# Optimization experiments

Hardware: AMD Instinct MI355X
Metric: run time of the kernel (lower is better)

Reference implementation:

```python
import jax, jax.numpy as jnp
import numpy as np

M, N, C, D = 2, 8, 1024, 256  # n_routers, num_adapters, channel_dim, down_sample_size
B, S = 32, 512


def setup_inputs() -> dict:
    key = jax.random.key(0)
    k1, k2, k3, k4, k5 = jax.random.split(key, 5)
    x = jax.random.normal(k1, (B, S, C), dtype=jnp.float32)
    expert_index = jax.random.randint(k2, (M, B), 0, N, dtype=jnp.int32)
    down_w = jax.random.normal(k3, (M, N, C, D), dtype=jnp.float32) * 0.01
    down_b = jax.random.normal(k4, (M, N, D), dtype=jnp.float32) * 0.01
    up_w = jax.random.normal(k5, (M, N, D, C), dtype=jnp.float32) * 0.01
    return {"x": x, "expert_index": expert_index, "down_w": down_w,
            "down_b": down_b, "up_w": up_w}


def reference(x, expert_index, down_w, down_b, up_w):
    # Gather per-(router, batch-element) adapter weights along the adapter axis.
    idx = expert_index  # [M, B]
    bw_down = jnp.take_along_axis(down_w, idx[:, :, None, None], axis=1)  # [M, B, C, D]
    bb_down = jnp.take_along_axis(down_b, idx[:, :, None], axis=1)        # [M, B, D]
    bw_up = jnp.take_along_axis(up_w, idx[:, :, None, None], axis=1)      # [M, B, D, C]
    # z = swish(x @ W_down + b_down)  -> [M, B, S, D]
    z = jnp.einsum('bsc,mbcd->mbsd', x, bw_down) + bb_down[:, :, None, :]
    z = jax.nn.silu(z)
    # u = z @ W_up -> [M, B, S, C]
    u = jnp.einsum('mbsd,mbdc->mbsc', z, bw_up)
    return u
```

## Files before the change

### kernel.cpp

```cpp
#include <hip/hip_runtime.h>
#include <stdint.h>

typedef unsigned short u16;
typedef __bf16 bf16x8 __attribute__((ext_vector_type(8)));
typedef float f32x4 __attribute__((ext_vector_type(4)));

#define MM 2
#define NN 8
#define CC 1024
#define DD 256
#define BB 32
#define SS 512

__device__ __forceinline__ u16 f2bf(float f) {
  uint32_t u = __float_as_uint(f);
  u += 0x7FFFu + ((u >> 16) & 1u);
  return (u16)(u >> 16);
}

__device__ __forceinline__ void async16(const void* g, void* l) {
  __builtin_amdgcn_global_load_lds(
      (const __attribute__((address_space(1))) uint32_t*)g,
      (__attribute__((address_space(3))) uint32_t*)l, 16, 0, 0);
}

__global__ __launch_bounds__(256) void cvt_f32_bf16(
    const float* __restrict__ in, u16* __restrict__ out, int n) {
  int i = (blockIdx.x * 256 + threadIdx.x) * 4;
  if (i >= n) return;
  float4 v = *reinterpret_cast<const float4*>(in + i);
  u16 o[4] = {f2bf(v.x), f2bf(v.y), f2bf(v.z), f2bf(v.w)};
  *reinterpret_cast<uint2*>(out + i) = *reinterpret_cast<const uint2*>(o);
}

__global__ __launch_bounds__(256) void transpose_cvt(
    const float* __restrict__ in, u16* __restrict__ out, int R, int L) {
  __shared__ float tile[32][33];
  const int slab = blockIdx.z;
  const float* src = in + (size_t)slab * R * L;
  u16* dst = out + (size_t)slab * R * L;
  const int c0 = blockIdx.x * 32;
  const int r0 = blockIdx.y * 32;
  const int tx = threadIdx.x & 31, ty = threadIdx.x >> 5;
#pragma unroll
  for (int i = 0; i < 32; i += 8)
    tile[ty + i][tx] = src[(size_t)(r0 + ty + i) * L + c0 + tx];
  __syncthreads();
#pragma unroll
  for (int i = 0; i < 32; i += 8)
    dst[(size_t)(c0 + ty + i) * R + r0 + tx] = f2bf(tile[tx][ty + i]);
}

__global__ __launch_bounds__(256) void gemm_down(
    const u16* __restrict__ xb, const u16* __restrict__ wdT,
    const float* __restrict__ db, const int* __restrict__ eidx,
    u16* __restrict__ z) {
  __shared__ __align__(16) u16 smA[128 * 32];
  __shared__ __align__(16) u16 smB[128 * 32];

  const int pair = blockIdx.z;
  const int m = pair >> 5;
  const int b = pair & 31;
  const int e = eidx[pair];
  const int s0 = blockIdx.y * 128;
  const int d0 = blockIdx.x * 128;

  const int tid = threadIdx.x;
  const int lane = tid & 63;
  const int wave = tid >> 6;
  const int quad = lane >> 4;
  const int l16 = lane & 15;

  const u16* Ab = xb + ((size_t)b * SS + s0) * CC;
  const u16* Bb = wdT + ((size_t)(m * NN + e) * DD + d0) * CC;

  const int r0r = (wave * 2 + 0) * 16 + (lane >> 2);
  const int r1r = (wave * 2 + 1) * 16 + (lane >> 2);
  const int kc = (lane & 3) * 8;
  const u16* gA0 = Ab + (size_t)r0r * CC + kc;
  const u16* gA1 = Ab + (size_t)r1r * CC + kc;
  const u16* gB0 = Bb + (size_t)r0r * CC + kc;
  const u16* gB1 = Bb + (size_t)r1r * CC + kc;
  u16* lA0 = smA + (wave * 2 + 0) * 512;
  u16* lA1 = smA + (wave * 2 + 1) * 512;
  u16* lB0 = smB + (wave * 2 + 0) * 512;
  u16* lB1 = smB + (wave * 2 + 1) * 512;

  const int wr = (wave >> 1) * 64;
  const int wc = (wave & 1) * 64;

  f32x4 acc[4][4];
#pragma unroll
  for (int i = 0; i < 4; ++i)
#pragma unroll
    for (int j = 0; j < 4; ++j) acc[i][j] = (f32x4){0.f, 0.f, 0.f, 0.f};

  for (int kk = 0; kk < CC; kk += 32) {
    async16(gA0 + kk, lA0);
    async16(gA1 + kk, lA1);
    async16(gB0 + kk, lB0);
    async16(gB1 + kk, lB1);
    __syncthreads();
    bf16x8 af[4], bfr[4];
#pragma unroll
    for (int i = 0; i < 4; ++i)
      af[i] = *reinterpret_cast<const bf16x8*>(&smA[(wr + i * 16 + l16) * 32 + quad * 8]);
#pragma unroll
    for (int j = 0; j < 4; ++j)
      bfr[j] = *reinterpret_cast<const bf16x8*>(&smB[(wc + j * 16 + l16) * 32 + quad * 8]);
#pragma unroll
    for (int i = 0; i < 4; ++i)
#pragma unroll
      for (int j = 0; j < 4; ++j)
        acc[i][j] = __builtin_amdgcn_mfma_f32_16x16x32_bf16(af[i], bfr[j], acc[i][j], 0, 0, 0);
    __syncthreads();
  }

  const float* bias_p = db + (size_t)(m * NN + e) * DD + d0;
  u16* zb = z + (size_t)pair * SS * DD;
#pragma unroll
  for (int j = 0; j < 4; ++j) {
    const int dloc = wc + j * 16 + l16;
    const float bias = bias_p[dloc];
#pragma unroll
    for (int i = 0; i < 4; ++i) {
      const int srow = s0 + wr + i * 16 + quad * 4;
#pragma unroll
      for (int r = 0; r < 4; ++r) {
        float v = acc[i][j][r] + bias;
        v = v / (1.f + __expf(-v));
        zb[(size_t)(srow + r) * DD + d0 + dloc] = f2bf(v);
      }
    }
  }
}

__global__ __launch_bounds__(256) void gemm_up(
    const u16* __restrict__ zb, const u16* __restrict__ wuT,
    const int* __restrict__ eidx, float* __restrict__ out) {
  __shared__ __align__(16) u16 smA[128 * 32];
  __shared__ __align__(16) u16 smB[128 * 32];

  const int pair = blockIdx.z;
  const int m = pair >> 5;
  const int e = eidx[pair];
  const int s0 = blockIdx.y * 128;
  const int c0 = blockIdx.x * 128;

  const int tid = threadIdx.x;
  const int lane = tid & 63;
  const int wave = tid >> 6;
  const int quad = lane >> 4;
  const int l16 = lane & 15;

  const u16* Ab = zb + ((size_t)pair * SS + s0) * DD;
  const u16* Bb = wuT + ((size_t)(m * NN + e) * CC + c0) * DD;

  const int r0r = (wave * 2 + 0) * 16 + (lane >> 2);
  const int r1r = (wave * 2 + 1) * 16 + (lane >> 2);
  const int kc = (lane & 3) * 8;
  const u16* gA0 = Ab + (size_t)r0r * DD + kc;
  const u16* gA1 = Ab + (size_t)r1r * DD + kc;
  const u16* gB0 = Bb + (size_t)r0r * DD + kc;
  const u16* gB1 = Bb + (size_t)r1r * DD + kc;
  u16* lA0 = smA + (wave * 2 + 0) * 512;
  u16* lA1 = smA + (wave * 2 + 1) * 512;
  u16* lB0 = smB + (wave * 2 + 0) * 512;
  u16* lB1 = smB + (wave * 2 + 1) * 512;

  const int wr = (wave >> 1) * 64;
  const int wc = (wave & 1) * 64;

  f32x4 acc[4][4];
#pragma unroll
  for (int i = 0; i < 4; ++i)
#pragma unroll
    for (int j = 0; j < 4; ++j) acc[i][j] = (f32x4){0.f, 0.f, 0.f, 0.f};

  for (int kk = 0; kk < DD; kk += 32) {
    async16(gA0 + kk, lA0);
    async16(gA1 + kk, lA1);
    async16(gB0 + kk, lB0);
    async16(gB1 + kk, lB1);
    __syncthreads();
    bf16x8 af[4], bfr[4];
#pragma unroll
    for (int i = 0; i < 4; ++i)
      af[i] = *reinterpret_cast<const bf16x8*>(&smA[(wr + i * 16 + l16) * 32 + quad * 8]);
#pragma unroll
    for (int j = 0; j < 4; ++j)
      bfr[j] = *reinterpret_cast<const bf16x8*>(&smB[(wc + j * 16 + l16) * 32 + quad * 8]);
#pragma unroll
    for (int i = 0; i < 4; ++i)
#pragma unroll
      for (int j = 0; j < 4; ++j)
        acc[i][j] = __builtin_amdgcn_mfma_f32_16x16x32_bf16(af[i], bfr[j], acc[i][j], 0, 0, 0);
    __syncthreads();
  }

  float* ob = out + (size_t)pair * SS * CC;
#pragma unroll
  for (int j = 0; j < 4; ++j) {
    const int cloc = c0 + wc + j * 16 + l16;
#pragma unroll
    for (int i = 0; i < 4; ++i) {
      const int srow = s0 + wr + i * 16 + quad * 4;
#pragma unroll
      for (int r = 0; r < 4; ++r)
        ob[(size_t)(srow + r) * CC + cloc] = acc[i][j][r];
    }
  }
}

extern "C" void kernel_launch(void* const* d_in, const int* in_sizes, int n_in,
                              void* d_out, int out_size, void* d_ws, size_t ws_size,
                              hipStream_t stream) {
  const float* x  = (const float*)d_in[0];
  const int* eidx = (const int*)d_in[1];
  const float* dw = (const float*)d_in[2];
  const float* db = (const float*)d_in[3];
  const float* uw = (const float*)d_in[4];
  float* out = (float*)d_out;

  char* ws = (char*)d_ws;
  u16* xb  = (u16*)(ws);
  u16* wdT = (u16*)(ws + (size_t)32 * 1024 * 1024);
  u16* wuT = (u16*)(ws + (size_t)40 * 1024 * 1024);
  u16* zb  = (u16*)(ws + (size_t)48 * 1024 * 1024);

  const int nx = BB * SS * CC;
  cvt_f32_bf16<<<dim3(nx / 4 / 256), dim3(256), 0, stream>>>(x, xb, nx);
  transpose_cvt<<<dim3(DD / 32, CC / 32, MM * NN), dim3(256), 0, stream>>>(dw, wdT, CC, DD);
  transpose_cvt<<<dim3(CC / 32, DD / 32, MM * NN), dim3(256), 0, stream>>>(uw, wuT, DD, CC);

  gemm_down<<<dim3(DD / 128, SS / 128, MM * BB), dim3(256), 0, stream>>>(xb, wdT, db, eidx, zb);
  gemm_up<<<dim3(CC / 128, SS / 128, MM * BB), dim3(256), 0, stream>>>(zb, wuT, eidx, out);
}
```

Baseline: 280.1 us.

## Fuse down and up adapter GEMMs in one kernel, merge prep kernels

```diff
diff --git a/kernel.cpp b/kernel.cpp
--- a/kernel.cpp
+++ b/kernel.cpp
@@ -24,23 +24,42 @@
       (__attribute__((address_space(3))) uint32_t*)l, 16, 0, 0);
 }
 
-__global__ __launch_bounds__(256) void cvt_f32_bf16(
-    const float* __restrict__ in, u16* __restrict__ out, int n) {
-  int i = (blockIdx.x * 256 + threadIdx.x) * 4;
-  if (i >= n) return;
-  float4 v = *reinterpret_cast<const float4*>(in + i);
-  u16 o[4] = {f2bf(v.x), f2bf(v.y), f2bf(v.z), f2bf(v.w)};
-  *reinterpret_cast<uint2*>(out + i) = *reinterpret_cast<const uint2*>(o);
-}
-
-__global__ __launch_bounds__(256) void transpose_cvt(
-    const float* __restrict__ in, u16* __restrict__ out, int R, int L) {
+#define CVT_BLOCKS 16384
+#define T_BLOCKS 4096
+__global__ __launch_bounds__(256) void prep(
+    const float* __restrict__ x, u16* __restrict__ xb,
+    const float* __restrict__ dw, u16* __restrict__ wdT,
+    const float* __restrict__ uw, u16* __restrict__ wuT) {
+  const int bid = blockIdx.x;
+  if (bid < CVT_BLOCKS) {
+    int i = (bid * 256 + threadIdx.x) * 4;
+    float4 v = *reinterpret_cast<const float4*>(x + i);
+    u16 o[4] = {f2bf(v.x), f2bf(v.y), f2bf(v.z), f2bf(v.w)};
+    *reinterpret_cast<uint2*>(xb + i) = *reinterpret_cast<const uint2*>(o);
+    return;
+  }
   __shared__ float tile[32][33];
-  const int slab = blockIdx.z;
-  const float* src = in + (size_t)slab * R * L;
-  u16* dst = out + (size_t)slab * R * L;
-  const int c0 = blockIdx.x * 32;
-  const int r0 = blockIdx.y * 32;
+  const float* src;
+  u16* dst;
+  int R, L, bx, by, slab;
+  if (bid < CVT_BLOCKS + T_BLOCKS) {
+    int t = bid - CVT_BLOCKS;
+    slab = t >> 8;
+    int t2 = t & 255;
+    bx = t2 & 7;  by = t2 >> 3;
+    R = CC; L = DD;
+    src = dw; dst = wdT;
+  } else {
+    int t = bid - CVT_BLOCKS - T_BLOCKS;
+    slab = t >> 8;
+    int t2 = t & 255;
+    bx = t2 & 31; by = t2 >> 5;
+    R = DD; L = CC;
+    src = uw; dst = wuT;
+  }
+  src += (size_t)slab * R * L;
+  dst += (size_t)slab * R * L;
+  const int c0 = bx * 32, r0 = by * 32;
   const int tx = threadIdx.x & 31, ty = threadIdx.x >> 5;
 #pragma unroll
   for (int i = 0; i < 32; i += 8)
@@ -51,19 +70,19 @@
     dst[(size_t)(c0 + ty + i) * R + r0 + tx] = f2bf(tile[tx][ty + i]);
 }
 
-__global__ __launch_bounds__(256) void gemm_down(
+__global__ __launch_bounds__(256) void fused_adapter(
     const u16* __restrict__ xb, const u16* __restrict__ wdT,
-    const float* __restrict__ db, const int* __restrict__ eidx,
-    u16* __restrict__ z) {
-  __shared__ __align__(16) u16 smA[128 * 32];
-  __shared__ __align__(16) u16 smB[128 * 32];
-
-  const int pair = blockIdx.z;
+    const u16* __restrict__ wuT, const float* __restrict__ db,
+    const int* __restrict__ eidx, float* __restrict__ out) {
+  __shared__ __align__(16) u16 smA[64 * 32];
+  __shared__ __align__(16) u16 smB[256 * 32];
+  __shared__ __align__(16) u16 zl[8 * 64 * 32];
+
+  const int pair = blockIdx.y;
   const int m = pair >> 5;
   const int b = pair & 31;
   const int e = eidx[pair];
-  const int s0 = blockIdx.y * 128;
-  const int d0 = blockIdx.x * 128;
+  const int s0 = blockIdx.x * 64;
 
   const int tid = threadIdx.x;
   const int lane = tid & 63;
@@ -71,23 +90,20 @@
   const int quad = lane >> 4;
   const int l16 = lane & 15;
 
+  const int srow = lane >> 2;
+  const int kc = (lane & 3) * 8;
+
   const u16* Ab = xb + ((size_t)b * SS + s0) * CC;
-  const u16* Bb = wdT + ((size_t)(m * NN + e) * DD + d0) * CC;
-
-  const int r0r = (wave * 2 + 0) * 16 + (lane >> 2);
-  const int r1r = (wave * 2 + 1) * 16 + (lane >> 2);
-  const int kc = (lane & 3) * 8;
-  const u16* gA0 = Ab + (size_t)r0r * CC + kc;
-  const u16* gA1 = Ab + (size_t)r1r * CC + kc;
-  const u16* gB0 = Bb + (size_t)r0r * CC + kc;
-  const u16* gB1 = Bb + (size_t)r1r * CC + kc;
-  u16* lA0 = smA + (wave * 2 + 0) * 512;
-  u16* lA1 = smA + (wave * 2 + 1) * 512;
-  u16* lB0 = smB + (wave * 2 + 0) * 512;
-  u16* lB1 = smB + (wave * 2 + 1) * 512;
-
-  const int wr = (wave >> 1) * 64;
-  const int wc = (wave & 1) * 64;
+  const u16* Bd = wdT + (size_t)(m * NN + e) * DD * CC;
+  const u16* gA = Ab + (size_t)(wave * 16 + srow) * CC + kc;
+  u16* lA = smA + wave * 16 * 32;
+  const u16* gB[4];
+  u16* lB[4];
+#pragma unroll
+  for (int t = 0; t < 4; ++t) {
+    gB[t] = Bd + (size_t)(t * 64 + wave * 16 + srow) * CC + kc;
+    lB[t] = smB + (t * 64 + wave * 16) * 32;
+  }
 
   f32x4 acc[4][4];
 #pragma unroll
@@ -96,18 +112,17 @@
     for (int j = 0; j < 4; ++j) acc[i][j] = (f32x4){0.f, 0.f, 0.f, 0.f};
 
   for (int kk = 0; kk < CC; kk += 32) {
-    async16(gA0 + kk, lA0);
-    async16(gA1 + kk, lA1);
-    async16(gB0 + kk, lB0);
-    async16(gB1 + kk, lB1);
+    async16(gA + kk, lA);
+#pragma unroll
+    for (int t = 0; t < 4; ++t) async16(gB[t] + kk, lB[t]);
     __syncthreads();
     bf16x8 af[4], bfr[4];
 #pragma unroll
     for (int i = 0; i < 4; ++i)
-      af[i] = *reinterpret_cast<const bf16x8*>(&smA[(wr + i * 16 + l16) * 32 + quad * 8]);
+      af[i] = *reinterpret_cast<const bf16x8*>(&smA[(i * 16 + l16) * 32 + quad * 8]);
 #pragma unroll
     for (int j = 0; j < 4; ++j)
-      bfr[j] = *reinterpret_cast<const bf16x8*>(&smB[(wc + j * 16 + l16) * 32 + quad * 8]);
+      bfr[j] = *reinterpret_cast<const bf16x8*>(&smB[(wave * 64 + j * 16 + l16) * 32 + quad * 8]);
 #pragma unroll
     for (int i = 0; i < 4; ++i)
 #pragma unroll
@@ -116,98 +131,70 @@
     __syncthreads();
   }
 
-  const float* bias_p = db + (size_t)(m * NN + e) * DD + d0;
-  u16* zb = z + (size_t)pair * SS * DD;
+  const float* bias_p = db + (size_t)(m * NN + e) * DD;
 #pragma unroll
   for (int j = 0; j < 4; ++j) {
-    const int dloc = wc + j * 16 + l16;
-    const float bias = bias_p[dloc];
+    const int d = wave * 64 + j * 16 + l16;
+    const float bias = bias_p[d];
+    const int kt = d >> 5;
+    const int kl = d & 31;
 #pragma unroll
     for (int i = 0; i < 4; ++i) {
-      const int srow = s0 + wr + i * 16 + quad * 4;
+      const int sr = i * 16 + quad * 4;
 #pragma unroll
       for (int r = 0; r < 4; ++r) {
         float v = acc[i][j][r] + bias;
         v = v / (1.f + __expf(-v));
-        zb[(size_t)(srow + r) * DD + d0 + dloc] = f2bf(v);
+        zl[(kt * 64 + sr + r) * 32 + kl] = f2bf(v);
       }
     }
   }
-}
-
-__global__ __launch_bounds__(256) void gemm_up(
-    const u16* __restrict__ zb, const u16* __restrict__ wuT,
-    const int* __restrict__ eidx, float* __restrict__ out) {
-  __shared__ __align__(16) u16 smA[128 * 32];
-  __shared__ __align__(16) u16 smB[128 * 32];
-
-  const int pair = blockIdx.z;
-  const int m = pair >> 5;
-  const int e = eidx[pair];
-  const int s0 = blockIdx.y * 128;
-  const int c0 = blockIdx.x * 128;
-
-  const int tid = threadIdx.x;
-  const int lane = tid & 63;
-  const int wave = tid >> 6;
-  const int quad = lane >> 4;
-  const int l16 = lane & 15;
-
-  const u16* Ab = zb + ((size_t)pair * SS + s0) * DD;
-  const u16* Bb = wuT + ((size_t)(m * NN + e) * CC + c0) * DD;
-
-  const int r0r = (wave * 2 + 0) * 16 + (lane >> 2);
-  const int r1r = (wave * 2 + 1) * 16 + (lane >> 2);
-  const int kc = (lane & 3) * 8;
-  const u16* gA0 = Ab + (size_t)r0r * DD + kc;
-  const u16* gA1 = Ab + (size_t)r1r * DD + kc;
-  const u16* gB0 = Bb + (size_t)r0r * DD + kc;
-  const u16* gB1 = Bb + (size_t)r1r * DD + kc;
-  u16* lA0 = smA + (wave * 2 + 0) * 512;
-  u16* lA1 = smA + (wave * 2 + 1) * 512;
-  u16* lB0 = smB + (wave * 2 + 0) * 512;
-  u16* lB1 = smB + (wave * 2 + 1) * 512;
-
-  const int wr = (wave >> 1) * 64;
-  const int wc = (wave & 1) * 64;
-
-  f32x4 acc[4][4];
-#pragma unroll
-  for (int i = 0; i < 4; ++i)
-#pragma unroll
-    for (int j = 0; j < 4; ++j) acc[i][j] = (f32x4){0.f, 0.f, 0.f, 0.f};
-
-  for (int kk = 0; kk < DD; kk += 32) {
-    async16(gA0 + kk, lA0);
-    async16(gA1 + kk, lA1);
-    async16(gB0 + kk, lB0);
-    async16(gB1 + kk, lB1);
-    __syncthreads();
-    bf16x8 af[4], bfr[4];
+  __syncthreads();
+
+  const u16* Bu = wuT + (size_t)(m * NN + e) * CC * DD;
+  float* ob = out + ((size_t)pair * SS + s0) * CC;
+
+  for (int ct = 0; ct < 4; ++ct) {
+    const u16* gB2[4];
+#pragma unroll
+    for (int t = 0; t < 4; ++t)
+      gB2[t] = Bu + (size_t)(ct * 256 + t * 64 + wave * 16 + srow) * DD + kc;
+
 #pragma unroll
     for (int i = 0; i < 4; ++i)
-      af[i] = *reinterpret_cast<const bf16x8*>(&smA[(wr + i * 16 + l16) * 32 + quad * 8]);
-#pragma unroll
-    for (int j = 0; j < 4; ++j)
-      bfr[j] = *reinterpret_cast<const bf16x8*>(&smB[(wc + j * 16 + l16) * 32 + quad * 8]);
-#pragma unroll
-    for (int i = 0; i < 4; ++i)
+#pragma unroll
+      for (int j = 0; j < 4; ++j) acc[i][j] = (f32x4){0.f, 0.f, 0.f, 0.f};
+
+    for (int kk = 0; kk < DD; kk += 32) {
+#pragma unroll
+      for (int t = 0; t < 4; ++t) async16(gB2[t] + kk, lB[t]);
+      __syncthreads();
+      bf16x8 af[4], bfr[4];
+      const int it = kk >> 5;
+#pragma unroll
+      for (int i = 0; i < 4; ++i)
+        af[i] = *reinterpret_cast<const bf16x8*>(&zl[(it * 64 + i * 16 + l16) * 32 + quad * 8]);
 #pragma unroll
       for (int j = 0; j < 4; ++j)
-        acc[i][j] = __builtin_amdgcn_mfma_f32_16x16x32_bf16(af[i], bfr[j], acc[i][j], 0, 0, 0);
-    __syncthreads();
-  }
-
-  float* ob = out + (size_t)pair * SS * CC;
-#pragma unroll
-  for (int j = 0; j < 4; ++j) {
-    const int cloc = c0 + wc + j * 16 + l16;
-#pragma unroll
-    for (int i = 0; i < 4; ++i) {
-      const int srow = s0 + wr + i * 16 + quad * 4;
-#pragma unroll
-      for (int r = 0; r < 4; ++r)
-        ob[(size_t)(srow + r) * CC + cloc] = acc[i][j][r];
+        bfr[j] = *reinterpret_cast<const bf16x8*>(&smB[(wave * 64 + j * 16 + l16) * 32 + quad * 8]);
+#pragma unroll
+      for (int i = 0; i < 4; ++i)
+#pragma unroll
+        for (int j = 0; j < 4; ++j)
+          acc[i][j] = __builtin_amdgcn_mfma_f32_16x16x32_bf16(af[i], bfr[j], acc[i][j], 0, 0, 0);
+      __syncthreads();
+    }
+
+#pragma unroll
+    for (int j = 0; j < 4; ++j) {
+      const int c = ct * 256 + wave * 64 + j * 16 + l16;
+#pragma unroll
+      for (int i = 0; i < 4; ++i) {
+        const int sr = i * 16 + quad * 4;
+#pragma unroll
+        for (int r = 0; r < 4; ++r)
+          ob[(size_t)(sr + r) * CC + c] = acc[i][j][r];
+      }
     }
   }
 }
@@ -226,13 +213,9 @@
   u16* xb  = (u16*)(ws);
   u16* wdT = (u16*)(ws + (size_t)32 * 1024 * 1024);
   u16* wuT = (u16*)(ws + (size_t)40 * 1024 * 1024);
-  u16* zb  = (u16*)(ws + (size_t)48 * 1024 * 1024);
-
-  const int nx = BB * SS * CC;
-  cvt_f32_bf16<<<dim3(nx / 4 / 256), dim3(256), 0, stream>>>(x, xb, nx);
-  transpose_cvt<<<dim3(DD / 32, CC / 32, MM * NN), dim3(256), 0, stream>>>(dw, wdT, CC, DD);
-  transpose_cvt<<<dim3(CC / 32, DD / 32, MM * NN), dim3(256), 0, stream>>>(uw, wuT, DD, CC);
-
-  gemm_down<<<dim3(DD / 128, SS / 128, MM * BB), dim3(256), 0, stream>>>(xb, wdT, db, eidx, zb);
-  gemm_up<<<dim3(CC / 128, SS / 128, MM * BB), dim3(256), 0, stream>>>(zb, wuT, eidx, out);
-}
+
+  prep<<<dim3(CVT_BLOCKS + 2 * T_BLOCKS), dim3(256), 0, stream>>>(
+      x, xb, dw, wdT, uw, wuT);
+  fused_adapter<<<dim3(SS / 64, MM * BB), dim3(256), 0, stream>>>(
+      xb, wdT, wuT, db, eidx, out);
+}
```

Result: no change. 275.6 us (-1.6%).
